# Kernel tuning notes

Measured on AMD Instinct MI355X. Metric: run time of the kernel, lower is better.

The kernel has to match this reference:

```python
import jax, jax.numpy as jnp
import numpy as np

NUM_ITER = 3  # Newton-Schulz iterations (init kwarg)

def setup_inputs() -> dict:
    key = jax.random.key(0)
    x = jax.random.normal(key, (64, 28, 28, 256), dtype=jnp.float32)
    return {"x": x}

def reference(x):
    B, H, W, C = x.shape
    n = H * W
    # Faithful to K.reshape(inputs, (batch, C, n)) -- a plain row-major reshape
    X = x.reshape(B, C, n)
    # Sigma = X @ I_hat @ X^T with I_hat = (1/n)(I - (1/n) 11^T), i.e. the
    # centering projector: identical to mean-centering then (1/n) Xc Xc^T.
    Xc = X - X.mean(axis=2, keepdims=True)            # [B, C, n]
    Sigma = jnp.einsum('bcn,bdn->bcd', Xc, Xc) / n    # [B, C, C]
    trace = jnp.trace(Sigma, axis1=1, axis2=2)[:, None, None]  # [B,1,1]
    A = Sigma / trace
    I = jnp.eye(C, dtype=x.dtype)
    I3 = 3.0 * I
    Y = A
    Z = jnp.broadcast_to(I, (B, C, C))
    # Newton-Schulz: NOTE original updates Z with the already-updated Y
    for _ in range(NUM_ITER):
        Y = 0.5 * jnp.matmul(Y, I3 - jnp.matmul(Z, Y))
        Z = 0.5 * jnp.matmul(I3 - jnp.matmul(Z, Y), Z)
    Cmat = jnp.sqrt(trace) * Y                        # [B, C, C]
    # Upper-triangular (incl. diagonal) vectorization, row-major order
    iu_r, iu_c = jnp.triu_indices(C)
    return Cmat[:, iu_r, iu_c]                        # [B, C*(C+1)/2]
```

## Files before the change

### kernel.cpp

```cpp
#include <hip/hip_runtime.h>
#include <math.h>

#define BATCH 64
#define CD 256
#define NX 784
#define TRIU_N 32896
#define MSZ 65536
#define REG_STRIDE 1032
#define ARR_STRIDE 4128
#define BUF_STRIDE 16512

typedef unsigned short ushort_t;
typedef unsigned int uint_t;
typedef __attribute__((ext_vector_type(8))) short short8;
typedef __attribute__((ext_vector_type(16))) float floatx16;

__device__ __forceinline__ void decode_bid(int bid, int& tile, int& bb) {
    int xcd = bid & 7, g = bid >> 3;
    tile = g & 3;
    bb = ((g >> 2) << 3) | xcd;
}

__device__ __forceinline__ float bf2f(ushort_t h) {
    return __uint_as_float(((uint_t)h) << 16);
}
__device__ __forceinline__ void pack2(float f0, float f1, uint_t& hp, uint_t& lp) {
    uint_t h, l;
    asm("v_cvt_pk_bf16_f32 %0, %1, %2" : "=v"(h) : "v"(f0), "v"(f1));
    float r0 = f0 - __uint_as_float(h << 16);
    float r1 = f1 - __uint_as_float(h & 0xffff0000u);
    asm("v_cvt_pk_bf16_f32 %0, %1, %2" : "=v"(l) : "v"(r0), "v"(r1));
    hp = h; lp = l;
}
__device__ __forceinline__ void store8(ushort_t* H, ushort_t* L, const float* y) {
    uint_t hw[4], lw[4];
    #pragma unroll
    for (int i = 0; i < 4; ++i) pack2(y[2*i], y[2*i+1], hw[i], lw[i]);
    *(uint4*)H = make_uint4(hw[0], hw[1], hw[2], hw[3]);
    *(uint4*)L = make_uint4(lw[0], lw[1], lw[2], lw[3]);
}

__device__ __forceinline__ int swoff(int r, int c) {
    int p = r >> 7, s = (c >> 5) & 7, ks = (c >> 4) & 1, kh = (c >> 3) & 1;
    return ((((p * 8 + s) * 2 + ks) * 2 + kh) * 128 + (r & 127)) * 8 + (c & 7);
}

__device__ __forceinline__ void rawbar() {
    __builtin_amdgcn_s_barrier();
    __builtin_amdgcn_sched_barrier(0);
}

__device__ __forceinline__ void gbar(unsigned* bars, int slot) {
    __syncthreads();
    if (threadIdx.x == 0) {
        __hip_atomic_fetch_add(&bars[slot], 1u, __ATOMIC_RELEASE, __HIP_MEMORY_SCOPE_AGENT);
        while (__hip_atomic_load(&bars[slot], __ATOMIC_RELAXED, __HIP_MEMORY_SCOPE_AGENT) < 4u)
            __builtin_amdgcn_s_sleep(4);
        __builtin_amdgcn_fence(__ATOMIC_ACQUIRE, "agent");
    }
    __syncthreads();
    __builtin_amdgcn_sched_barrier(0);
}

__device__ __forceinline__ void mfma_stage8(const ushort_t* us, int bufbase,
                                            int wr, int wcp, int khalf, int lrow,
                                            floatx16* acc) {
    __builtin_amdgcn_s_setprio(1);
    #pragma unroll
    for (int ks = 0; ks < 2; ++ks) {
        const int rid = ks * 2 + khalf;
        const ushort_t* rb = us + bufbase + rid * REG_STRIDE + lrow * 8;
        short8 aH = *(const short8*)(rb + wr * 256);
        short8 aL = *(const short8*)(rb + ARR_STRIDE + wr * 256);
        #pragma unroll
        for (int cq = 0; cq < 2; ++cq) {
            const int col = wcp * 2 + cq;
            short8 bH = *(const short8*)(rb + 2 * ARR_STRIDE + col * 256);
            short8 bL = *(const short8*)(rb + 3 * ARR_STRIDE + col * 256);
            acc[cq] = __builtin_amdgcn_mfma_f32_32x32x16_bf16(aH, bH, acc[cq], 0, 0, 0);
            acc[cq] = __builtin_amdgcn_mfma_f32_32x32x16_bf16(aH, bL, acc[cq], 0, 0, 0);
            acc[cq] = __builtin_amdgcn_mfma_f32_32x32x16_bf16(aL, bH, acc[cq], 0, 0, 0);
        }
    }
    __builtin_amdgcn_s_setprio(0);
}

__device__ __forceinline__ void acc_bounce(float* fsmem, const floatx16* acc,
                                           int wr, int wcp, int khalf, int lrow) {
    __syncthreads();
    #pragma unroll
    for (int cq = 0; cq < 2; ++cq)
        #pragma unroll
        for (int i = 0; i < 16; ++i) {
            int rl = (i & 3) + ((i >> 2) << 3) + (khalf << 2);
            fsmem[(wr * 32 + rl) * 129 + (wcp * 2 + cq) * 32 + lrow] = acc[cq][i];
        }
    __syncthreads();
}

struct Cur { float4 v[2][2]; };

__device__ __forceinline__ void gr_load(const float* Xb, int rowBase, int colBase, int s,
                                        const int* side, const int* srow, const int* skq,
                                        Cur& c) {
    #pragma unroll
    for (int q = 0; q < 2; ++q) {
        int gk = s * 32 + skq[q] * 8;
        if (gk < NX) {
            const float* p = Xb + (size_t)((side[q] ? colBase : rowBase) + srow[q]) * NX + gk;
            c.v[q][0] = *(const float4*)p;
            c.v[q][1] = *(const float4*)(p + 4);
        } else {
            c.v[q][0] = make_float4(0.f, 0.f, 0.f, 0.f);
            c.v[q][1] = make_float4(0.f, 0.f, 0.f, 0.f);
        }
    }
}

__device__ __forceinline__ void gr_conv(ushort_t* us, int bufbase, const Cur& c,
                                        const int* side, const int* srow, const int* skq,
                                        float* rs) {
    #pragma unroll
    for (int q = 0; q < 2; ++q) {
        float f[8] = {c.v[q][0].x, c.v[q][0].y, c.v[q][0].z, c.v[q][0].w,
                      c.v[q][1].x, c.v[q][1].y, c.v[q][1].z, c.v[q][1].w};
        rs[q] += ((f[0] + f[1]) + (f[2] + f[3])) + ((f[4] + f[5]) + (f[6] + f[7]));
        uint_t hp[4], lp[4];
        #pragma unroll
        for (int i = 0; i < 4; ++i) pack2(f[2*i], f[2*i+1], hp[i], lp[i]);
        int base = bufbase + (side[q] * 2) * ARR_STRIDE + skq[q] * REG_STRIDE + srow[q] * 8;
        *(uint4*)(us + base)              = make_uint4(hp[0], hp[1], hp[2], hp[3]);
        *(uint4*)(us + base + ARR_STRIDE) = make_uint4(lp[0], lp[1], lp[2], lp[3]);
    }
}

__device__ __forceinline__ void gram_phase(float* fsmem, const float* __restrict__ X,
                                           float* __restrict__ means, float* __restrict__ tr,
                                           ushort_t* __restrict__ Gh, ushort_t* __restrict__ Gl,
                                           int tile, int bb) {
    ushort_t* us = (ushort_t*)fsmem;
    float* dsh = fsmem + 16512;
    const int rowBase = (tile >> 1) * 128, colBase = (tile & 1) * 128;
    const int tid = threadIdx.x, lane = tid & 63, wv = tid >> 6;
    const int wr = wv >> 1, wcp = wv & 1;
    const int khalf = lane >> 5, lrow = lane & 31;
    const float* Xb = X + (size_t)bb * CD * NX;

    floatx16 acc[2];
    #pragma unroll
    for (int cq = 0; cq < 2; ++cq)
        #pragma unroll
        for (int i = 0; i < 16; ++i) acc[cq][i] = 0.f;

    int side[2], srow[2], skq[2];
    #pragma unroll
    for (int q = 0; q < 2; ++q) {
        int gid = q * 512 + tid;
        side[q] = gid >> 9;
        srow[q] = (gid >> 2) & 127;
        skq[q]  = gid & 3;
    }
    float rs[2] = {0.f, 0.f};

    Cur curA, curB;
    gr_load(Xb, rowBase, colBase, 0, side, srow, skq, curA);
    gr_load(Xb, rowBase, colBase, 1, side, srow, skq, curB);
    gr_conv(us, 0, curA, side, srow, skq, rs);

    for (int s = 0; s < 25; s += 2) {
        asm volatile("s_waitcnt lgkmcnt(0)" ::: "memory");
        rawbar();
        if (s + 2 <= 24) gr_load(Xb, rowBase, colBase, s + 2, side, srow, skq, curA);
        mfma_stage8(us, 0, wr, wcp, khalf, lrow, acc);
        if (s + 1 <= 24) gr_conv(us, BUF_STRIDE, curB, side, srow, skq, rs);
        if (s + 1 <= 24) {
            asm volatile("s_waitcnt lgkmcnt(0)" ::: "memory");
            rawbar();
            if (s + 3 <= 24) gr_load(Xb, rowBase, colBase, s + 3, side, srow, skq, curB);
            mfma_stage8(us, BUF_STRIDE, wr, wcp, khalf, lrow, acc);
            gr_conv(us, 0, curA, side, srow, skq, rs);
        }
    }

    {
        float r0 = rs[0], r1 = rs[1];
        r0 += __shfl_xor(r0, 1, 64); r0 += __shfl_xor(r0, 2, 64);
        r1 += __shfl_xor(r1, 1, 64); r1 += __shfl_xor(r1, 2, 64);
        if ((tid & 3) == 0) {
            int rr = tid >> 2;
            means[bb * CD + rowBase + rr] = r0 * (1.0f / NX);
            means[bb * CD + colBase + rr] = r1 * (1.0f / NX);
        }
    }

    acc_bounce(fsmem, acc, wr, wcp, khalf, lrow);
    const int rloc = tid & 127;
    const int r = rowBase + rloc;
    const float mr = means[bb * CD + r];
    const bool diagblk = (rowBase == colBase);
    float dv = 0.f;
    #pragma unroll
    for (int gi = 0; gi < 4; ++gi) {
        int g = (tid >> 7) + gi * 4;
        int c0 = colBase + g * 8;
        int so = swoff(r, c0);
        float v[8];
        #pragma unroll
        for (int j = 0; j < 8; ++j) {
            v[j] = fsmem[rloc * 129 + g * 8 + j] * (1.0f / NX) - mr * means[bb * CD + c0 + j];
            if (diagblk && (c0 + j) == r) dv += v[j];
        }
        store8(Gh + (size_t)bb * MSZ + so, Gl + (size_t)bb * MSZ + so, v);
    }
    if (diagblk) {
        for (int off = 32; off; off >>= 1) dv += __shfl_down(dv, off, 64);
        if (lane == 0) dsh[wv] = dv;
        __syncthreads();
        if (tid == 0) {
            float s = ((dsh[0] + dsh[1]) + (dsh[2] + dsh[3]))
                    + ((dsh[4] + dsh[5]) + (dsh[6] + dsh[7]));
            atomicAdd(&tr[bb], s);
        }
    }
}

__device__ __forceinline__ void ns_prefetch(const ushort_t* const* arrp, ushort_t* us,
                                            int wv, int lane, int s, int buf) {
    #pragma unroll
    for (int j = 0; j < 4; ++j) {
        int ck = wv * 4 + j;
        int arr = ck >> 3, rid = (ck >> 1) & 3, half = ck & 1;
        const ushort_t* g = arrp[arr] + s * 4096 + rid * 1024 + half * 512 + lane * 8;
        ushort_t* l = us + buf * BUF_STRIDE + arr * ARR_STRIDE + rid * REG_STRIDE + half * 512;
        __builtin_amdgcn_global_load_lds(
            (const __attribute__((address_space(1))) unsigned int*)g,
            (__attribute__((address_space(3))) unsigned int*)l, 16, 0, 0);
    }
}

template<int MODE>
__device__ __forceinline__ void ns_phase(float* fsmem, int tile, int bb,
    const ushort_t* __restrict__ Ah, const ushort_t* __restrict__ Al,
    const ushort_t* __restrict__ Bh, const ushort_t* __restrict__ Bl,
    const ushort_t* __restrict__ Mh, const ushort_t* __restrict__ Ml,
    float it, float st,
    ushort_t* __restrict__ O1h, ushort_t* __restrict__ O1l,
    ushort_t* __restrict__ O2h, ushort_t* __restrict__ O2l,
    float* __restrict__ outT) {
    const int rowBase = (tile >> 1) * 128, colBase = (tile & 1) * 128;
    if (MODE == 3 && rowBase > colBase) return;
    __syncthreads();
    ushort_t* us = (ushort_t*)fsmem;
    const size_t mb = (size_t)bb * MSZ;
    const int tid = threadIdx.x, lane = tid & 63, wv = tid >> 6;
    const int wr = wv >> 1, wcp = wv & 1;
    const int khalf = lane >> 5, lrow = lane & 31;
    const ushort_t* arrp[4] = {
        Ah + mb + (size_t)(rowBase >> 7) * 32768,
        Al + mb + (size_t)(rowBase >> 7) * 32768,
        Bh + mb + (size_t)(colBase >> 7) * 32768,
        Bl + mb + (size_t)(colBase >> 7) * 32768 };

    floatx16 acc[2];
    #pragma unroll
    for (int cq = 0; cq < 2; ++cq)
        #pragma unroll
        for (int i = 0; i < 16; ++i) acc[cq][i] = 0.f;

    ns_prefetch(arrp, us, wv, lane, 0, 0);
    ns_prefetch(arrp, us, wv, lane, 1, 1);
    ns_prefetch(arrp, us, wv, lane, 2, 2);
    #pragma unroll
    for (int s = 0; s < 8; ++s) {
        if (s <= 5)      asm volatile("s_waitcnt vmcnt(8)" ::: "memory");
        else if (s == 6) asm volatile("s_waitcnt vmcnt(4)" ::: "memory");
        else             asm volatile("s_waitcnt vmcnt(0)" ::: "memory");
        rawbar();
        mfma_stage8(us, (s & 3) * BUF_STRIDE, wr, wcp, khalf, lrow, acc);
        if (s < 5) ns_prefetch(arrp, us, wv, lane, s + 3, (s + 3) & 3);
    }

    acc_bounce(fsmem, acc, wr, wcp, khalf, lrow);
    const int rloc = tid & 127;
    const int r = rowBase + rloc;
    #pragma unroll
    for (int gi = 0; gi < 4; ++gi) {
        int g = (tid >> 7) + gi * 4;
        int c0 = colBase + g * 8;
        int so = swoff(r, c0);
        float v[8];
        #pragma unroll
        for (int j = 0; j < 8; ++j) v[j] = fsmem[rloc * 129 + g * 8 + j];
        if (MODE == 0) {
            store8(O1h + mb + so, O1l + mb + so, v);
        } else {
            float mv[8];
            {
                uint4 mh4 = *(const uint4*)(Mh + mb + so);
                uint4 ml4 = *(const uint4*)(Ml + mb + so);
                const uint_t mhw[4] = {mh4.x, mh4.y, mh4.z, mh4.w};
                const uint_t mlw[4] = {ml4.x, ml4.y, ml4.z, ml4.w};
                #pragma unroll
                for (int i = 0; i < 4; ++i) {
                    mv[2*i]   = __uint_as_float(mhw[i] << 16) + __uint_as_float(mlw[i] << 16);
                    mv[2*i+1] = __uint_as_float(mhw[i] & 0xffff0000u) + __uint_as_float(mlw[i] & 0xffff0000u);
                }
            }
            if (MODE == 1) {
                float y[8];
                #pragma unroll
                for (int j = 0; j < 8; ++j) y[j] = fmaf(1.5f, mv[j], -0.5f * v[j]);
                store8(O1h + mb + so, O1l + mb + so, y);
            } else if (MODE == 2) {
                float y[8], z[8];
                #pragma unroll
                for (int j = 0; j < 8; ++j) {
                    y[j] = 1.5f * it * mv[j] - 0.5f * it * it * v[j];
                    z[j] = ((r == c0 + j) ? 1.5f : 0.f) - 0.5f * y[j];
                }
                store8(O1h + mb + so, O1l + mb + so, y);
                store8(O2h + mb + so, O2l + mb + so, z);
            } else if (MODE == 4) {
                float w[8];
                #pragma unroll
                for (int j = 0; j < 8; ++j)
                    w[j] = ((r == c0 + j) ? 2.25f : 0.f) - 1.5f * mv[j] + 0.25f * v[j];
                store8(O1h + mb + so, O1l + mb + so, v);
                store8(O2h + mb + so, O2l + mb + so, w);
            } else {
                int tb = r * CD - (r * (r - 1)) / 2 - r;
                #pragma unroll
                for (int j = 0; j < 8; ++j) {
                    float y = fmaf(1.5f, mv[j], -0.5f * v[j]);
                    int c = c0 + j;
                    if (c >= r) outT[(size_t)bb * TRIU_N + tb + c] = st * y;
                }
            }
        }
    }
}

__global__ __launch_bounds__(512, 1)
void fused_all(const float* __restrict__ X,
               ushort_t* __restrict__ S0h, ushort_t* __restrict__ S0l,
               ushort_t* __restrict__ S1h, ushort_t* __restrict__ S1l,
               ushort_t* __restrict__ S2h, ushort_t* __restrict__ S2l,
               ushort_t* __restrict__ S3h, ushort_t* __restrict__ S3l,
               ushort_t* __restrict__ S4h, ushort_t* __restrict__ S4l,
               float* __restrict__ means, float* __restrict__ tr,
               float* __restrict__ outT, unsigned* __restrict__ bars) {
    __shared__ __align__(16) float fsmem[33024];
    int tile, bb;
    decode_bid(blockIdx.x, tile, bb);

    gram_phase(fsmem, X, means, tr, S0h, S0l, tile, bb);
    gbar(bars, bb * 8 + 0);

    const float trv = tr[bb];
    const float it = 1.0f / trv, st = sqrtf(trv);

    ns_phase<2>(fsmem, tile, bb, S0h, S0l, S0h, S0l, S0h, S0l, it, 0.f,
                S1h, S1l, S2h, S2l, nullptr);
    gbar(bars, bb * 8 + 1);
    ns_phase<4>(fsmem, tile, bb, S1h, S1l, S1h, S1l, S1h, S1l, 0.f, 0.f,
                S3h, S3l, S0h, S0l, nullptr);
    gbar(bars, bb * 8 + 2);
    ns_phase<1>(fsmem, tile, bb, S2h, S2l, S3h, S3l, S1h, S1l, 0.f, 0.f,
                S4h, S4l, nullptr, nullptr, nullptr);
    gbar(bars, bb * 8 + 3);
    ns_phase<1>(fsmem, tile, bb, S0h, S0l, S4h, S4l, S2h, S2l, 0.f, 0.f,
                S1h, S1l, nullptr, nullptr, nullptr);
    ns_phase<0>(fsmem, tile, bb, S4h, S4l, S4h, S4l, nullptr, nullptr, 0.f, 0.f,
                S3h, S3l, nullptr, nullptr, nullptr);
    gbar(bars, bb * 8 + 4);
    ns_phase<3>(fsmem, tile, bb, S1h, S1l, S3h, S3l, S4h, S4l, 0.f, st,
                nullptr, nullptr, nullptr, nullptr, outT);
}

extern "C" void kernel_launch(void* const* d_in, const int* in_sizes, int n_in,
                              void* d_out, int out_size, void* d_ws, size_t ws_size,
                              hipStream_t stream) {
    const float* x = (const float*)d_in[0];
    float* out = (float*)d_out;
    char* ws = (char*)d_ws;
    const size_t HS = (size_t)BATCH * MSZ * 2;
    ushort_t* S0h = (ushort_t*)(ws + 0 * HS);
    ushort_t* S0l = (ushort_t*)(ws + 1 * HS);
    ushort_t* S1h = (ushort_t*)(ws + 2 * HS);
    ushort_t* S1l = (ushort_t*)(ws + 3 * HS);
    ushort_t* S2h = (ushort_t*)(ws + 4 * HS);
    ushort_t* S2l = (ushort_t*)(ws + 5 * HS);
    ushort_t* S3h = (ushort_t*)(ws + 6 * HS);
    ushort_t* S3l = (ushort_t*)(ws + 7 * HS);
    ushort_t* S4h = (ushort_t*)(ws + 8 * HS);
    ushort_t* S4l = (ushort_t*)(ws + 9 * HS);
    float* means = (float*)(ws + 10 * HS);
    float* tr = means + BATCH * CD;
    unsigned* bars = (unsigned*)(tr + BATCH);

    hipMemsetAsync(tr, 0, BATCH * sizeof(float) + BATCH * 8 * sizeof(unsigned), stream);
    fused_all<<<256, 512, 0, stream>>>(x, S0h, S0l, S1h, S1l, S2h, S2l,
                                       S3h, S3l, S4h, S4l, means, tr, out, bars);
}
```

Before: 220.3 us.

## Split persistent fused kernel into four launches at barrier boundaries

Replaces three of the five per-batch software grid barriers in the single persistent kernel with kernel launch boundaries, producing four kernels. Stream ordering between launches now provides the synchronization that the atomic spin barriers gave, and the barrier counter array shrinks accordingly. This removes spin-wait and atomic traffic and may help with scheduling or register allocation in the smaller kernels. In exchange it adds launch overhead and removes any chance of overlap between batches that are in different phases.

```diff
diff --git a/kernel.cpp b/kernel.cpp
--- a/kernel.cpp
+++ b/kernel.cpp
@@ -341,38 +341,63 @@
 }
 
 __global__ __launch_bounds__(512, 1)
-void fused_all(const float* __restrict__ X,
-               ushort_t* __restrict__ S0h, ushort_t* __restrict__ S0l,
-               ushort_t* __restrict__ S1h, ushort_t* __restrict__ S1l,
-               ushort_t* __restrict__ S2h, ushort_t* __restrict__ S2l,
-               ushort_t* __restrict__ S3h, ushort_t* __restrict__ S3l,
-               ushort_t* __restrict__ S4h, ushort_t* __restrict__ S4l,
-               float* __restrict__ means, float* __restrict__ tr,
-               float* __restrict__ outT, unsigned* __restrict__ bars) {
+void fused_k1(const float* __restrict__ X,
+              ushort_t* __restrict__ S0h, ushort_t* __restrict__ S0l,
+              ushort_t* __restrict__ S1h, ushort_t* __restrict__ S1l,
+              ushort_t* __restrict__ S2h, ushort_t* __restrict__ S2l,
+              float* __restrict__ means, float* __restrict__ tr,
+              unsigned* __restrict__ bars) {
     __shared__ __align__(16) float fsmem[33024];
     int tile, bb;
     decode_bid(blockIdx.x, tile, bb);
-
     gram_phase(fsmem, X, means, tr, S0h, S0l, tile, bb);
-    gbar(bars, bb * 8 + 0);
-
-    const float trv = tr[bb];
-    const float it = 1.0f / trv, st = sqrtf(trv);
-
+    gbar(bars, bb * 2 + 0);
+    const float it = 1.0f / tr[bb];
     ns_phase<2>(fsmem, tile, bb, S0h, S0l, S0h, S0l, S0h, S0l, it, 0.f,
                 S1h, S1l, S2h, S2l, nullptr);
-    gbar(bars, bb * 8 + 1);
+}
+
+__global__ __launch_bounds__(512, 1)
+void fused_k2(const ushort_t* __restrict__ S1h, const ushort_t* __restrict__ S1l,
+              const ushort_t* __restrict__ S2h, const ushort_t* __restrict__ S2l,
+              ushort_t* __restrict__ S3h, ushort_t* __restrict__ S3l,
+              ushort_t* __restrict__ S0h, ushort_t* __restrict__ S0l,
+              ushort_t* __restrict__ S4h, ushort_t* __restrict__ S4l,
+              unsigned* __restrict__ bars) {
+    __shared__ __align__(16) float fsmem[33024];
+    int tile, bb;
+    decode_bid(blockIdx.x, tile, bb);
     ns_phase<4>(fsmem, tile, bb, S1h, S1l, S1h, S1l, S1h, S1l, 0.f, 0.f,
                 S3h, S3l, S0h, S0l, nullptr);
-    gbar(bars, bb * 8 + 2);
+    gbar(bars, bb * 2 + 1);
     ns_phase<1>(fsmem, tile, bb, S2h, S2l, S3h, S3l, S1h, S1l, 0.f, 0.f,
                 S4h, S4l, nullptr, nullptr, nullptr);
-    gbar(bars, bb * 8 + 3);
+}
+
+__global__ __launch_bounds__(512, 1)
+void fused_k3(const ushort_t* __restrict__ S0h, const ushort_t* __restrict__ S0l,
+              const ushort_t* __restrict__ S4h, const ushort_t* __restrict__ S4l,
+              const ushort_t* __restrict__ S2h, const ushort_t* __restrict__ S2l,
+              ushort_t* __restrict__ S1h, ushort_t* __restrict__ S1l,
+              ushort_t* __restrict__ S3h, ushort_t* __restrict__ S3l) {
+    __shared__ __align__(16) float fsmem[33024];
+    int tile, bb;
+    decode_bid(blockIdx.x, tile, bb);
     ns_phase<1>(fsmem, tile, bb, S0h, S0l, S4h, S4l, S2h, S2l, 0.f, 0.f,
                 S1h, S1l, nullptr, nullptr, nullptr);
     ns_phase<0>(fsmem, tile, bb, S4h, S4l, S4h, S4l, nullptr, nullptr, 0.f, 0.f,
                 S3h, S3l, nullptr, nullptr, nullptr);
-    gbar(bars, bb * 8 + 4);
+}
+
+__global__ __launch_bounds__(512, 1)
+void fused_k4(const ushort_t* __restrict__ S1h, const ushort_t* __restrict__ S1l,
+              const ushort_t* __restrict__ S3h, const ushort_t* __restrict__ S3l,
+              const ushort_t* __restrict__ S4h, const ushort_t* __restrict__ S4l,
+              const float* __restrict__ tr, float* __restrict__ outT) {
+    __shared__ __align__(16) float fsmem[33024];
+    int tile, bb;
+    decode_bid(blockIdx.x, tile, bb);
+    const float st = sqrtf(tr[bb]);
     ns_phase<3>(fsmem, tile, bb, S1h, S1l, S3h, S3l, S4h, S4l, 0.f, st,
                 nullptr, nullptr, nullptr, nullptr, outT);
 }
@@ -398,7 +423,9 @@
     float* tr = means + BATCH * CD;
     unsigned* bars = (unsigned*)(tr + BATCH);
 
-    hipMemsetAsync(tr, 0, BATCH * sizeof(float) + BATCH * 8 * sizeof(unsigned), stream);
-    fused_all<<<256, 512, 0, stream>>>(x, S0h, S0l, S1h, S1l, S2h, S2l,
-                                       S3h, S3l, S4h, S4l, means, tr, out, bars);
-}
+    hipMemsetAsync(tr, 0, BATCH * sizeof(float) + BATCH * 2 * sizeof(unsigned), stream);
+    fused_k1<<<256, 512, 0, stream>>>(x, S0h, S0l, S1h, S1l, S2h, S2l, means, tr, bars);
+    fused_k2<<<256, 512, 0, stream>>>(S1h, S1l, S2h, S2l, S3h, S3l, S0h, S0l, S4h, S4l, bars);
+    fused_k3<<<256, 512, 0, stream>>>(S0h, S0l, S4h, S4l, S2h, S2l, S1h, S1l, S3h, S3l);
+    fused_k4<<<256, 512, 0, stream>>>(S1h, S1l, S3h, S3l, S4h, S4l, tr, out);
+}
```

After: 214.0 us. 2.9% less time.
